# Kernel tuning notes

Hardware: AMD Instinct MI355X
Metric: run time of the kernel (lower is better)

Reference implementation:

```python
import jax, jax.numpy as jnp
import numpy as np

EPS_DIAG = 1e-4
EPS_SOFT = 1e-5
SCALE_DIV = 100000.0


def _cov2cor(x):
    # x: [N, C, d, d]; scale rows and cols by 1/sqrt(|diag|) (== D^-1 @ x @ D^-1)
    dia = jnp.abs(jnp.diagonal(x, axis1=-2, axis2=-1))          # [N, C, d]
    inv = 1.0 / jnp.sqrt(jnp.maximum(dia, EPS_DIAG))
    cor = x * inv[..., :, None] * inv[..., None, :]
    return jnp.clip(cor, -1.0, 1.0)


def _soft_pd_max(x):
    # x: [N, C, d, d]
    x = x - jnp.max(x, axis=(2, 3), keepdims=True)
    e = jnp.exp(x)
    dia = jnp.sum(e, axis=-1)                                    # [N, C, d]
    dia = jnp.maximum(dia, jnp.sum(dia, axis=2, keepdims=True) / SCALE_DIV)
    dia = jnp.maximum(dia, EPS_SOFT)
    inv = 1.0 / jnp.sqrt(dia)
    return e * inv[..., :, None] * inv[..., None, :]


def setup_inputs() -> dict:
    key = jax.random.key(0)
    k0, k1, k2, k3 = jax.random.split(key, 4)
    N, C, d = 64, 64, 64
    inputs = jax.random.normal(k0, (N, C, d, d), dtype=jnp.float32)
    # NonNeg uniform [0, 2/C] init for queries/keys
    w_queries = jax.random.uniform(k1, (C, C), dtype=jnp.float32, minval=0.0, maxval=2.0 / C)
    w_keys = jax.random.uniform(k2, (C, C), dtype=jnp.float32, minval=0.0, maxval=2.0 / C)
    # values: |N(0, 1/sqrt(C))| column-L1-normalized
    wv = jnp.abs(jax.random.normal(k3, (C, C), dtype=jnp.float32) / jnp.sqrt(jnp.float32(C)))
    w_values = wv / jnp.sum(wv, axis=0)
    return {"inputs": inputs, "w_queries": w_queries, "w_keys": w_keys, "w_values": w_values}


def reference(inputs, w_queries, w_keys, w_values):
    cor = _cov2cor(inputs)                                       # [N, C, d, d]
    X = jnp.transpose(cor, (0, 2, 3, 1))                         # [N, d, d, C]
    XWQ = jnp.matmul(X, w_queries)                               # [N, d, d, C]
    XWK = jnp.matmul(X, w_keys)
    XWV = jnp.matmul(X, w_values)
    XWQt = jnp.transpose(XWQ, (0, 3, 1, 2))                      # [N, C, d, d]
    XWKt = jnp.transpose(XWK, (0, 3, 2, 1))                      # [N, C, d, d] (transposed within dxd)
    XWKT = jnp.transpose(XWK, (0, 3, 1, 2))
    A_pre = jnp.matmul(jnp.matmul(XWKt, XWQt), XWKT)             # [N, C, d, d]
    A = _soft_pd_max(A_pre)
    V = jnp.transpose(XWV, (0, 3, 1, 2))                         # [N, C, d, d]
    AXA = jnp.matmul(jnp.matmul(A, V), jnp.transpose(A, (0, 1, 3, 2)))
    return inputs + AXA
```

## Files before the change

### kernel.cpp

```cpp
#include <hip/hip_runtime.h>

#define PITCH 72

typedef __attribute__((ext_vector_type(8))) short short8v;
typedef __attribute__((ext_vector_type(4))) short short4v;
typedef __attribute__((ext_vector_type(4))) float f32x4;

__device__ __forceinline__ short f2bf(float v) {
    unsigned u = __builtin_bit_cast(unsigned, v);
    unsigned r = (u + 0x7FFFu + ((u >> 16) & 1u)) >> 16;
    return (short)r;
}
__device__ __forceinline__ float bf2f(short s) {
    unsigned u = ((unsigned)(unsigned short)s) << 16;
    return __builtin_bit_cast(float, u);
}

#define MFMA(a, b, c) __builtin_amdgcn_mfma_f32_16x16x32_bf16(a, b, c, 0, 0, 0)

__device__ __forceinline__ short8v ldfrag(const short* p, int rowtile, int kc, int l) {
    return *(const short8v*)&p[(rowtile * 16 + (l & 15)) * PITCH + kc * 32 + (l >> 4) * 8];
}
__device__ __forceinline__ short8v gfrag(const short* __restrict__ p, int rowtile, int kc, int l) {
    return *(const short8v*)&p[(rowtile * 16 + (l & 15)) * 64 + kc * 32 + (l >> 4) * 8];
}

__device__ __forceinline__ void p1(const short* xh, const short* yh,
                                   int w, int l, f32x4 (&acc)[4]) {
#pragma unroll
    for (int ct = 0; ct < 4; ++ct) acc[ct] = (f32x4){0.f, 0.f, 0.f, 0.f};
#pragma unroll
    for (int kc = 0; kc < 2; ++kc) {
        short8v aH = ldfrag(xh, w, kc, l);
#pragma unroll
        for (int ct = 0; ct < 4; ++ct)
            acc[ct] = MFMA(aH, ldfrag(yh, ct, kc, l), acc[ct]);
    }
}

__device__ __forceinline__ void p1_g(const short* __restrict__ xg, const short* yh,
                                     int w, int l, f32x4 (&acc)[4]) {
#pragma unroll
    for (int ct = 0; ct < 4; ++ct) acc[ct] = (f32x4){0.f, 0.f, 0.f, 0.f};
#pragma unroll
    for (int kc = 0; kc < 2; ++kc) {
        short8v aH = gfrag(xg, w, kc, l);
#pragma unroll
        for (int ct = 0; ct < 4; ++ct)
            acc[ct] = MFMA(aH, ldfrag(yh, ct, kc, l), acc[ct]);
    }
}

__device__ __forceinline__ void p2v_g(const short* __restrict__ xg,
                                      const short* yh, const short* yl,
                                      int w, int l, f32x4 (&acc)[4]) {
#pragma unroll
    for (int ct = 0; ct < 4; ++ct) acc[ct] = (f32x4){0.f, 0.f, 0.f, 0.f};
#pragma unroll
    for (int kc = 0; kc < 2; ++kc) {
        short8v aH = gfrag(xg, w, kc, l);
#pragma unroll
        for (int ct = 0; ct < 4; ++ct) {
            acc[ct] = MFMA(aH, ldfrag(yh, ct, kc, l), acc[ct]);
            acc[ct] = MFMA(aH, ldfrag(yl, ct, kc, l), acc[ct]);
        }
    }
}

__device__ __forceinline__ void p2a(const short* xh, const short* xl,
                                    const short* yh,
                                    int w, int l, f32x4 (&acc)[4]) {
#pragma unroll
    for (int ct = 0; ct < 4; ++ct) acc[ct] = (f32x4){0.f, 0.f, 0.f, 0.f};
#pragma unroll
    for (int kc = 0; kc < 2; ++kc) {
        short8v aH = ldfrag(xh, w, kc, l);
        short8v aL = ldfrag(xl, w, kc, l);
#pragma unroll
        for (int ct = 0; ct < 4; ++ct) {
            short8v bH = ldfrag(yh, ct, kc, l);
            acc[ct] = MFMA(aH, bH, acc[ct]);
            acc[ct] = MFMA(aL, bH, acc[ct]);
        }
    }
}

__device__ __forceinline__ void pack1(const f32x4 (&acc)[4], short* zh, int w, int l) {
    int m0 = w * 16 + (l >> 4) * 4;
#pragma unroll
    for (int ct = 0; ct < 4; ++ct) {
        int n = ct * 16 + (l & 15);
        short4v h;
#pragma unroll
        for (int r = 0; r < 4; ++r) h[r] = f2bf(acc[ct][r]);
        *(short4v*)&zh[n * PITCH + m0] = h;
    }
}

__device__ __forceinline__ void idtrans_ip1(short* pa, int w, int l) {
    short8v a0 = ldfrag(pa, w, 0, l);
    short8v a1 = ldfrag(pa, w, 1, l);
    short8v I0, I1;
#pragma unroll
    for (int j = 0; j < 8; ++j) {
        int bit = 8 * (l >> 4) + j;
        I0[j] = (bit == (l & 15))      ? (short)0x3F80 : (short)0;
        I1[j] = (bit == (l & 15) + 16) ? (short)0x3F80 : (short)0;
    }
    __syncthreads();
    int m0 = w * 16 + (l >> 4) * 4;
    const f32x4 z4 = {0.f, 0.f, 0.f, 0.f};
#pragma unroll
    for (int s = 0; s < 4; ++s) {
        f32x4 d = MFMA((s >> 1) ? a1 : a0, (s & 1) ? I1 : I0, z4);
        short4v ha;
#pragma unroll
        for (int r = 0; r < 4; ++r) ha[r] = f2bf(d[r]);
        *(short4v*)&pa[(s * 16 + (l & 15)) * PITCH + m0] = ha;
    }
}

__global__ __launch_bounds__(256) void k0_invdiag(const float* __restrict__ x,
                                                  float* __restrict__ invd) {
    int t = blockIdx.x * 256 + threadIdx.x;
    int nc = t >> 6, k = t & 63;
    float v = fabsf(x[(size_t)nc * 4096 + (size_t)k * 65]);
    invd[t] = rsqrtf(fmaxf(v, 1e-4f));
}

__global__ __launch_bounds__(256) void k0b_w3(const float* __restrict__ wq,
                                              const float* __restrict__ wk,
                                              const float* __restrict__ wv,
                                              short* __restrict__ w3h) {
    int idx = blockIdx.x * 256 + threadIdx.x;
    int co = idx >> 6, c = idx & 63;
    const float* w = (co < 64) ? wq : (co < 128) ? wk : wv;
    w3h[idx] = f2bf(w[c * 64 + (co & 63)]);
}

__global__ __launch_bounds__(256, 5) void k1_mix_mfma(
    const float* __restrict__ x, const float* __restrict__ invd,
    const short* __restrict__ w3h,
    short* __restrict__ Qh, short* __restrict__ Kh, short* __restrict__ Vh)
{
    __shared__ __align__(16) short zbuf[13824];
    short* ch = zbuf;

    const int b = blockIdx.x, n = b >> 6, i = b & 63;
    const int t = threadIdx.x, l = t & 63, w = t >> 6;
    const size_t nbase = (size_t)n * 64;

#pragma unroll
    for (int rep = 0; rep < 4; ++rep) {
        int id = rep * 256 + t;
        int c = id >> 4, j4 = (id & 15) * 4;
        float4 xv = *(const float4*)&x[((nbase + c) * 64 + i) * 64 + j4];
        float ii = invd[(nbase + c) * 64 + i];
        float4 jv = *(const float4*)&invd[(nbase + c) * 64 + j4];
        float vv[4] = {xv.x * ii * jv.x, xv.y * ii * jv.y,
                       xv.z * ii * jv.z, xv.w * ii * jv.w};
        short4v h;
#pragma unroll
        for (int r = 0; r < 4; ++r)
            h[r] = f2bf(fminf(1.0f, fmaxf(-1.0f, vv[r])));
        *(short4v*)&ch[c * PITCH + j4] = h;
    }
    __syncthreads();
    idtrans_ip1(ch, w, l);
    __syncthreads();

    f32x4 acc[4][3];
#pragma unroll
    for (int jt = 0; jt < 4; ++jt)
#pragma unroll
        for (int cc = 0; cc < 3; ++cc) acc[jt][cc] = (f32x4){0.f, 0.f, 0.f, 0.f};
#pragma unroll
    for (int kc = 0; kc < 2; ++kc) {
#pragma unroll
        for (int cc = 0; cc < 3; ++cc) {
            short8v bH = gfrag(w3h, w * 3 + cc, kc, l);
#pragma unroll
            for (int jt = 0; jt < 4; ++jt) {
                short8v aH = ldfrag(ch, jt, kc, l);
                acc[jt][cc] = MFMA(aH, bH, acc[jt][cc]);
            }
        }
    }
    __syncthreads();

    {
        int m0 = (l >> 4) * 4, nb = l & 15;
#pragma unroll
        for (int cc = 0; cc < 3; ++cc) {
            int nrow = (w * 3 + cc) * 16 + nb;
#pragma unroll
            for (int jt = 0; jt < 4; ++jt) {
                short4v h;
#pragma unroll
                for (int r = 0; r < 4; ++r) h[r] = f2bf(acc[jt][cc][r]);
                *(short4v*)&zbuf[nrow * PITCH + jt * 16 + m0] = h;
            }
        }
    }
    __syncthreads();

#pragma unroll
    for (int rep = 0; rep < 12; ++rep) {
        int id = rep * 256 + t;
        int row = id >> 4, j4 = (id & 15) * 4;
        short4v v = *(short4v*)&zbuf[row * PITCH + j4];
        if (rep < 4) {
            *(short4v*)&Qh[(nbase + row) * 4096 + (size_t)i * 64 + j4] = v;
        } else if (rep < 8) {
            *(short4v*)&Kh[(nbase + row - 64) * 4096 + (size_t)i * 64 + j4] = v;
        } else {
            *(short4v*)&Vh[(nbase + row - 128) * 4096 + (size_t)i * 64 + j4] = v;
        }
    }
}

__global__ __launch_bounds__(256, 5) void k2_attn_mfma(
    const float* __restrict__ x,
    const short* __restrict__ Qh, const short* __restrict__ Kh,
    const short* __restrict__ Vh,
    float* __restrict__ out)
{
    __shared__ __align__(16) short P[3][4608];
    __shared__ float part[4][64];
    __shared__ float invs[64];
    __shared__ float red[4];

    const int t = threadIdx.x, l = t & 63, w = t >> 6;
    const int nc = blockIdx.x;
    const size_t gbase = (size_t)nc * 4096;

    const short* qh = Qh + gbase;
    const short* kh = Kh + gbase;
    const short* vh = Vh + gbase;

#pragma unroll
    for (int rep = 0; rep < 4; ++rep) {
        int id = rep * 256 + t;
        int r = id >> 4, c4 = (id & 15) * 4;
        *(short4v*)&P[0][r * PITCH + c4] = *(const short4v*)&kh[r * 64 + c4];
    }
    __syncthreads();

    idtrans_ip1(P[0], w, l);
    __syncthreads();

    f32x4 acc[4];

    p1_g(qh, P[0], w, l, acc);
    pack1(acc, P[1], w, l);
    __syncthreads();

    p1(P[1], P[0], w, l, acc);

    float mx = -1e30f;
#pragma unroll
    for (int ct = 0; ct < 4; ++ct)
#pragma unroll
        for (int r = 0; r < 4; ++r) mx = fmaxf(mx, acc[ct][r]);
#pragma unroll
    for (int off = 1; off < 64; off <<= 1) mx = fmaxf(mx, __shfl_xor(mx, off));
    if (l == 0) red[w] = mx;
    __syncthreads();
    mx = fmaxf(fmaxf(red[0], red[1]), fmaxf(red[2], red[3]));

    float e[4][4];
    float cs[4];
#pragma unroll
    for (int ct = 0; ct < 4; ++ct) {
        float s = 0.f;
#pragma unroll
        for (int r = 0; r < 4; ++r) {
            float ev = __expf(acc[ct][r] - mx);
            e[ct][r] = ev;
            s += ev;
        }
        cs[ct] = s;
    }
#pragma unroll
    for (int ct = 0; ct < 4; ++ct) {
        cs[ct] += __shfl_xor(cs[ct], 16);
        cs[ct] += __shfl_xor(cs[ct], 32);
    }
    if (l < 16) {
#pragma unroll
        for (int ct = 0; ct < 4; ++ct) part[w][ct * 16 + l] = cs[ct];
    }
    __syncthreads();
    if (t < 64) {
        float dia = part[0][t] + part[1][t] + part[2][t] + part[3][t];
        float tot = dia;
#pragma unroll
        for (int off = 1; off < 64; off <<= 1) tot += __shfl_xor(tot, off);
        dia = fmaxf(dia, tot / 100000.0f);
        dia = fmaxf(dia, 1e-5f);
        invs[t] = rsqrtf(dia);
    }
    __syncthreads();

    {
        int m0 = w * 16 + (l >> 4) * 4;
        float ir[4] = {invs[m0], invs[m0 + 1], invs[m0 + 2], invs[m0 + 3]};
        int nb = l & 15;
#pragma unroll
        for (int ct = 0; ct < 4; ++ct) {
            float ic = invs[ct * 16 + nb];
            short4v h, lo;
#pragma unroll
            for (int r = 0; r < 4; ++r) {
                float v = e[ct][r] * ir[r] * ic;
                short hb = f2bf(v);
                h[r]  = hb;
                lo[r] = f2bf(v - bf2f(hb));
            }
            *(short4v*)&P[1][(ct * 16 + nb) * PITCH + m0] = h;
            *(short4v*)&P[0][(ct * 16 + nb) * PITCH + m0] = lo;
        }
    }
    __syncthreads();

    p2v_g(vh, P[1], P[0], w, l, acc);
    pack1(acc, P[2], w, l);
    __syncthreads();

    p2a(P[1], P[0], P[2], w, l, acc);
    __syncthreads();

    {
        float* ofs = (float*)&P[0][0];
        int m0 = w * 16 + (l >> 4) * 4;
        int nb = l & 15;
#pragma unroll
        for (int ct = 0; ct < 4; ++ct)
#pragma unroll
            for (int r = 0; r < 4; ++r)
                ofs[(m0 + r) * 68 + ct * 16 + nb] = acc[ct][r];
    }
    __syncthreads();
    {
        const float* ofs = (const float*)&P[0][0];
#pragma unroll
        for (int rep = 0; rep < 4; ++rep) {
            int id = rep * 256 + t;
            int row = id >> 4, c4 = (id & 15) * 4;
            float4 v  = *(const float4*)&ofs[row * 68 + c4];
            float4 xv = *(const float4*)&x[gbase + (size_t)row * 64 + c4];
            *(float4*)&out[gbase + (size_t)row * 64 + c4] =
                make_float4(xv.x + v.x, xv.y + v.y, xv.z + v.z, xv.w + v.w);
        }
    }
}

extern "C" void kernel_launch(void* const* d_in, const int* in_sizes, int n_in,
                              void* d_out, int out_size, void* d_ws, size_t ws_size,
                              hipStream_t stream) {
    const float* x  = (const float*)d_in[0];
    const float* wq = (const float*)d_in[1];
    const float* wk = (const float*)d_in[2];
    const float* wv = (const float*)d_in[3];
    float* out = (float*)d_out;

    char* wsb = (char*)d_ws;
    float* invd = (float*)wsb;
    short* w3h  = (short*)(wsb + (1 << 20));
    short* Qh   = (short*)(wsb + (2 << 20));
    short* Kh   = Qh + 16777216;
    short* Vh   = Kh + 16777216;

    k0_invdiag<<<1024, 256, 0, stream>>>(x, invd);
    k0b_w3<<<48, 256, 0, stream>>>(wq, wk, wv, w3h);
    k1_mix_mfma<<<4096, 256, 0, stream>>>(x, invd, w3h, Qh, Kh, Vh);
    k2_attn_mfma<<<4096, 256, 0, stream>>>(x, Qh, Kh, Vh, out);
}
```

Baseline: 88.02 us.

## Process two rows per block in channel-mix kernel to reuse weight fragments

The channel-mixing kernel now handles two i-rows per block, halving the grid. Each weight fragment loaded from global memory feeds MFMAs for both rows, and output stores widen from 4 to 8 bf16 elements per thread. In exchange the block uses more shared memory and twice the accumulator registers, so the occupancy hint drops from 5 to 3 blocks per CU.

After: 92.88 us. 5.5% more time.

```diff
diff --git a/kernel.cpp b/kernel.cpp
--- a/kernel.cpp
+++ b/kernel.cpp
@@ -1,6 +1,7 @@
 #include <hip/hip_runtime.h>
 
 #define PITCH 72
+#define ZP 136
 
 typedef __attribute__((ext_vector_type(8))) short short8v;
 typedef __attribute__((ext_vector_type(4))) short short4v;
@@ -117,6 +118,34 @@
 #pragma unroll
         for (int r = 0; r < 4; ++r) ha[r] = f2bf(d[r]);
         *(short4v*)&pa[(s * 16 + (l & 15)) * PITCH + m0] = ha;
+    }
+}
+
+__device__ __forceinline__ void idtrans_ip2(short* pa, short* pb, int w, int l) {
+    short8v a0 = ldfrag(pa, w, 0, l);
+    short8v a1 = ldfrag(pa, w, 1, l);
+    short8v b0 = ldfrag(pb, w, 0, l);
+    short8v b1 = ldfrag(pb, w, 1, l);
+    short8v I0, I1;
+#pragma unroll
+    for (int j = 0; j < 8; ++j) {
+        int bit = 8 * (l >> 4) + j;
+        I0[j] = (bit == (l & 15))      ? (short)0x3F80 : (short)0;
+        I1[j] = (bit == (l & 15) + 16) ? (short)0x3F80 : (short)0;
+    }
+    __syncthreads();
+    int m0 = w * 16 + (l >> 4) * 4;
+    const f32x4 z4 = {0.f, 0.f, 0.f, 0.f};
+#pragma unroll
+    for (int s = 0; s < 4; ++s) {
+        f32x4 d = MFMA((s >> 1) ? a1 : a0, (s & 1) ? I1 : I0, z4);
+        f32x4 e = MFMA((s >> 1) ? b1 : b0, (s & 1) ? I1 : I0, z4);
+        short4v ha, hb2;
+#pragma unroll
+        for (int r = 0; r < 4; ++r) { ha[r] = f2bf(d[r]); hb2[r] = f2bf(e[r]); }
+        int drow = s * 16 + (l & 15);
+        *(short4v*)&pa[drow * PITCH + m0] = ha;
+        *(short4v*)&pb[drow * PITCH + m0] = hb2;
     }
 }
 
@@ -138,22 +167,26 @@
     w3h[idx] = f2bf(w[c * 64 + (co & 63)]);
 }
 
-__global__ __launch_bounds__(256, 5) void k1_mix_mfma(
+__global__ __launch_bounds__(256, 3) void k1_mix_mfma(
     const float* __restrict__ x, const float* __restrict__ invd,
     const short* __restrict__ w3h,
     short* __restrict__ Qh, short* __restrict__ Kh, short* __restrict__ Vh)
 {
-    __shared__ __align__(16) short zbuf[13824];
-    short* ch = zbuf;
-
-    const int b = blockIdx.x, n = b >> 6, i = b & 63;
+    __shared__ __align__(16) short smem[192 * ZP];
+    short* ch0 = smem;
+    short* ch1 = smem + 4608;
+
+    const int b = blockIdx.x, n = b >> 5, ip = b & 31;
     const int t = threadIdx.x, l = t & 63, w = t >> 6;
     const size_t nbase = (size_t)n * 64;
-
-#pragma unroll
-    for (int rep = 0; rep < 4; ++rep) {
+    const int i0 = ip * 2;
+
+#pragma unroll
+    for (int rep = 0; rep < 8; ++rep) {
         int id = rep * 256 + t;
-        int c = id >> 4, j4 = (id & 15) * 4;
+        int isel = id >> 10, rem = id & 1023;
+        int c = rem >> 4, j4 = (rem & 15) * 4;
+        int i = i0 + isel;
         float4 xv = *(const float4*)&x[((nbase + c) * 64 + i) * 64 + j4];
         float ii = invd[(nbase + c) * 64 + i];
         float4 jv = *(const float4*)&invd[(nbase + c) * 64 + j4];
@@ -163,26 +196,36 @@
 #pragma unroll
         for (int r = 0; r < 4; ++r)
             h[r] = f2bf(fminf(1.0f, fmaxf(-1.0f, vv[r])));
-        *(short4v*)&ch[c * PITCH + j4] = h;
-    }
-    __syncthreads();
-    idtrans_ip1(ch, w, l);
-    __syncthreads();
-
-    f32x4 acc[4][3];
+        short* dst = isel ? ch1 : ch0;
+        *(short4v*)&dst[c * PITCH + j4] = h;
+    }
+    __syncthreads();
+    idtrans_ip2(ch0, ch1, w, l);
+    __syncthreads();
+
+    f32x4 a0[4][3], a1[4][3];
 #pragma unroll
     for (int jt = 0; jt < 4; ++jt)
 #pragma unroll
-        for (int cc = 0; cc < 3; ++cc) acc[jt][cc] = (f32x4){0.f, 0.f, 0.f, 0.f};
+        for (int cc = 0; cc < 3; ++cc) {
+            a0[jt][cc] = (f32x4){0.f, 0.f, 0.f, 0.f};
+            a1[jt][cc] = (f32x4){0.f, 0.f, 0.f, 0.f};
+        }
 #pragma unroll
     for (int kc = 0; kc < 2; ++kc) {
+        short8v f0[4], f1[4];
+#pragma unroll
+        for (int jt = 0; jt < 4; ++jt) {
+            f0[jt] = ldfrag(ch0, jt, kc, l);
+            f1[jt] = ldfrag(ch1, jt, kc, l);
+        }
 #pragma unroll
         for (int cc = 0; cc < 3; ++cc) {
             short8v bH = gfrag(w3h, w * 3 + cc, kc, l);
 #pragma unroll
             for (int jt = 0; jt < 4; ++jt) {
-                short8v aH = ldfrag(ch, jt, kc, l);
-                acc[jt][cc] = MFMA(aH, bH, acc[jt][cc]);
+                a0[jt][cc] = MFMA(f0[jt], bH, a0[jt][cc]);
+                a1[jt][cc] = MFMA(f1[jt], bH, a1[jt][cc]);
             }
         }
     }
@@ -195,10 +238,14 @@
             int nrow = (w * 3 + cc) * 16 + nb;
 #pragma unroll
             for (int jt = 0; jt < 4; ++jt) {
-                short4v h;
-#pragma unroll
-                for (int r = 0; r < 4; ++r) h[r] = f2bf(acc[jt][cc][r]);
-                *(short4v*)&zbuf[nrow * PITCH + jt * 16 + m0] = h;
+                short4v h0, h1;
+#pragma unroll
+                for (int r = 0; r < 4; ++r) {
+                    h0[r] = f2bf(a0[jt][cc][r]);
+                    h1[r] = f2bf(a1[jt][cc][r]);
+                }
+                *(short4v*)&smem[nrow * ZP + jt * 16 + m0]      = h0;
+                *(short4v*)&smem[nrow * ZP + 64 + jt * 16 + m0] = h1;
             }
         }
     }
@@ -207,14 +254,15 @@
 #pragma unroll
     for (int rep = 0; rep < 12; ++rep) {
         int id = rep * 256 + t;
-        int row = id >> 4, j4 = (id & 15) * 4;
-        short4v v = *(short4v*)&zbuf[row * PITCH + j4];
+        int row = id >> 4, c8 = (id & 15) * 8;
+        short8v v = *(short8v*)&smem[row * ZP + c8];
+        size_t off = (size_t)i0 * 64 + c8;
         if (rep < 4) {
-            *(short4v*)&Qh[(nbase + row) * 4096 + (size_t)i * 64 + j4] = v;
+            *(short8v*)&Qh[(nbase + row) * 4096 + off] = v;
         } else if (rep < 8) {
-            *(short4v*)&Kh[(nbase + row - 64) * 4096 + (size_t)i * 64 + j4] = v;
+            *(short8v*)&Kh[(nbase + row - 64) * 4096 + off] = v;
         } else {
-            *(short4v*)&Vh[(nbase + row - 128) * 4096 + (size_t)i * 64 + j4] = v;
+            *(short8v*)&Vh[(nbase + row - 128) * 4096 + off] = v;
         }
     }
 }
@@ -373,6 +421,6 @@
 
     k0_invdiag<<<1024, 256, 0, stream>>>(x, invd);
     k0b_w3<<<48, 256, 0, stream>>>(wq, wk, wv, w3h);
-    k1_mix_mfma<<<4096, 256, 0, stream>>>(x, invd, w3h, Qh, Kh, Vh);
+    k1_mix_mfma<<<2048, 256, 0, stream>>>(x, invd, w3h, Qh, Kh, Vh);
     k2_attn_mfma<<<4096, 256, 0, stream>>>(x, Qh, Kh, Vh, out);
 }
```

## Store Q/K/V intermediates in block-contiguous layout for coalesced writes

Applied to the files above, without the earlier changes.

The mixing kernel now writes its whole 192x64 bf16 tile for each (n,i) block contiguously into one interleaved QKV buffer, using 16-byte stores, instead of scattering 8-byte rows across three separate [N,C,d,d] tensors. The attention kernel reads Q/K/V through a strided view (row stride 12288) to match. The aim is fully coalesced writes in the producer. The cost is that each row the consumer loads is now 128 bytes sitting 24KB away from the next, which may hurt read locality in k2.

After: 79.71 us. 1.1x faster.

```diff
diff --git a/kernel.cpp b/kernel.cpp
--- a/kernel.cpp
+++ b/kernel.cpp
@@ -1,6 +1,7 @@
 #include <hip/hip_runtime.h>
 
 #define PITCH 72
+#define QKV_STRIDE 12288
 
 typedef __attribute__((ext_vector_type(8))) short short8v;
 typedef __attribute__((ext_vector_type(4))) short short4v;
@@ -24,6 +25,10 @@
 __device__ __forceinline__ short8v gfrag(const short* __restrict__ p, int rowtile, int kc, int l) {
     return *(const short8v*)&p[(rowtile * 16 + (l & 15)) * 64 + kc * 32 + (l >> 4) * 8];
 }
+__device__ __forceinline__ short8v gfrag_s(const short* __restrict__ p, int rowtile,
+                                           int kc, int l, int stride) {
+    return *(const short8v*)&p[(rowtile * 16 + (l & 15)) * stride + kc * 32 + (l >> 4) * 8];
+}
 
 __device__ __forceinline__ void p1(const short* xh, const short* yh,
                                    int w, int l, f32x4 (&acc)[4]) {
@@ -44,7 +49,7 @@
     for (int ct = 0; ct < 4; ++ct) acc[ct] = (f32x4){0.f, 0.f, 0.f, 0.f};
 #pragma unroll
     for (int kc = 0; kc < 2; ++kc) {
-        short8v aH = gfrag(xg, w, kc, l);
+        short8v aH = gfrag_s(xg, w, kc, l, QKV_STRIDE);
 #pragma unroll
         for (int ct = 0; ct < 4; ++ct)
             acc[ct] = MFMA(aH, ldfrag(yh, ct, kc, l), acc[ct]);
@@ -58,7 +63,7 @@
     for (int ct = 0; ct < 4; ++ct) acc[ct] = (f32x4){0.f, 0.f, 0.f, 0.f};
 #pragma unroll
     for (int kc = 0; kc < 2; ++kc) {
-        short8v aH = gfrag(xg, w, kc, l);
+        short8v aH = gfrag_s(xg, w, kc, l, QKV_STRIDE);
 #pragma unroll
         for (int ct = 0; ct < 4; ++ct) {
             acc[ct] = MFMA(aH, ldfrag(yh, ct, kc, l), acc[ct]);
@@ -141,7 +146,7 @@
 __global__ __launch_bounds__(256, 5) void k1_mix_mfma(
     const float* __restrict__ x, const float* __restrict__ invd,
     const short* __restrict__ w3h,
-    short* __restrict__ Qh, short* __restrict__ Kh, short* __restrict__ Vh)
+    short* __restrict__ QKV)
 {
     __shared__ __align__(16) short zbuf[13824];
     short* ch = zbuf;
@@ -204,25 +209,20 @@
     }
     __syncthreads();
 
-#pragma unroll
-    for (int rep = 0; rep < 12; ++rep) {
-        int id = rep * 256 + t;
-        int row = id >> 4, j4 = (id & 15) * 4;
-        short4v v = *(short4v*)&zbuf[row * PITCH + j4];
-        if (rep < 4) {
-            *(short4v*)&Qh[(nbase + row) * 4096 + (size_t)i * 64 + j4] = v;
-        } else if (rep < 8) {
-            *(short4v*)&Kh[(nbase + row - 64) * 4096 + (size_t)i * 64 + j4] = v;
-        } else {
-            *(short4v*)&Vh[(nbase + row - 128) * 4096 + (size_t)i * 64 + j4] = v;
+    {
+        short* dst = QKV + (size_t)b * QKV_STRIDE;
+#pragma unroll
+        for (int rep = 0; rep < 6; ++rep) {
+            int id = rep * 256 + t;
+            int row = id >> 3, col = (id & 7) * 8;
+            *(short8v*)&dst[id * 8] = *(short8v*)&zbuf[row * PITCH + col];
         }
     }
 }
 
 __global__ __launch_bounds__(256, 5) void k2_attn_mfma(
     const float* __restrict__ x,
-    const short* __restrict__ Qh, const short* __restrict__ Kh,
-    const short* __restrict__ Vh,
+    const short* __restrict__ QKV,
     float* __restrict__ out)
 {
     __shared__ __align__(16) short P[3][4608];
@@ -231,18 +231,19 @@
     __shared__ float red[4];
 
     const int t = threadIdx.x, l = t & 63, w = t >> 6;
-    const int nc = blockIdx.x;
+    const int nc = blockIdx.x, n = nc >> 6, c = nc & 63;
     const size_t gbase = (size_t)nc * 4096;
 
-    const short* qh = Qh + gbase;
-    const short* kh = Kh + gbase;
-    const short* vh = Vh + gbase;
+    const short* qh = QKV + (size_t)n * 64 * QKV_STRIDE + (size_t)c * 64;
+    const short* kh = qh + 64 * 64;
+    const short* vh = qh + 128 * 64;
 
 #pragma unroll
     for (int rep = 0; rep < 4; ++rep) {
         int id = rep * 256 + t;
         int r = id >> 4, c4 = (id & 15) * 4;
-        *(short4v*)&P[0][r * PITCH + c4] = *(const short4v*)&kh[r * 64 + c4];
+        *(short4v*)&P[0][r * PITCH + c4] =
+            *(const short4v*)&kh[r * QKV_STRIDE + c4];
     }
     __syncthreads();
 
@@ -367,12 +368,10 @@
     char* wsb = (char*)d_ws;
     float* invd = (float*)wsb;
     short* w3h  = (short*)(wsb + (1 << 20));
-    short* Qh   = (short*)(wsb + (2 << 20));
-    short* Kh   = Qh + 16777216;
-    short* Vh   = Kh + 16777216;
+    short* QKV  = (short*)(wsb + (2 << 20));
 
     k0_invdiag<<<1024, 256, 0, stream>>>(x, invd);
     k0b_w3<<<48, 256, 0, stream>>>(wq, wk, wv, w3h);
-    k1_mix_mfma<<<4096, 256, 0, stream>>>(x, invd, w3h, Qh, Kh, Vh);
-    k2_attn_mfma<<<4096, 256, 0, stream>>>(x, Qh, Kh, Vh, out);
-}
+    k1_mix_mfma<<<4096, 256, 0, stream>>>(x, invd, w3h, QKV);
+    k2_attn_mfma<<<4096, 256, 0, stream>>>(x, QKV, out);
+}
```
